# Performance work log

Hardware: AMD Instinct MI355X
Metric: run time of the kernel (lower is better)

The kernel has to match this reference:

```python
import jax, jax.numpy as jnp
import numpy as np

BN_EPS = 1e-5
K = 3  # k_size


def _unfold(x, k):
    # torch F.unfold with padding=k//2, stride=1, viewed as (B, C, k*k, H, W).
    # Kernel positions are row-major (i slow, j fast), matching torch layout.
    p = k // 2
    B, C, H, W = x.shape
    xp = jnp.pad(x, ((0, 0), (0, 0), (p, p), (p, p)))
    pats = jnp.stack([xp[:, :, i:i + H, j:j + W]
                      for i in range(k) for j in range(k)], axis=2)
    return pats  # (B, C, k*k, H, W)


def _conv1x1(x, w, b):
    # w: (C_out, C_in), x: (B, C_in, H, W)
    return jnp.einsum('oc,bchw->bohw', w, x) + b[None, :, None, None]


def _bn(x, gamma, beta, mean, var):
    inv = gamma / jnp.sqrt(var + BN_EPS)
    return x * inv[None, :, None, None] + (beta - mean * inv)[None, :, None, None]


def setup_inputs() -> dict:
    key = jax.random.key(0)
    ks = jax.random.split(key, 12)
    B, C, H, W = 8, 256, 64, 64
    s = lambda k_, *sh: jax.random.normal(k_, sh, dtype=jnp.float32) * 0.05
    return {
        'x': jax.random.normal(ks[0], (B, C, H, W), dtype=jnp.float32),
        # feature_embedding: Conv2d(C, C, 1) + BN
        'w_embed': s(ks[1], C, C), 'b_embed': jnp.zeros((C,), jnp.float32),
        'bn1_gamma': jnp.ones((C,), jnp.float32), 'bn1_beta': jnp.zeros((C,), jnp.float32),
        'bn1_mean': jnp.zeros((C,), jnp.float32), 'bn1_var': jnp.ones((C,), jnp.float32),
        # enhance: Conv2d(2C, C, 1) + BN
        'w_enh': s(ks[2], C, 2 * C), 'b_enh': jnp.zeros((C,), jnp.float32),
        'bn2_gamma': jnp.ones((C,), jnp.float32), 'bn2_beta': jnp.zeros((C,), jnp.float32),
        'bn2_mean': jnp.zeros((C,), jnp.float32), 'bn2_var': jnp.ones((C,), jnp.float32),
        # weight_gen: Conv2d(2C, C//4, 1) -> ReLU -> Conv2d(C//4, C, 1) -> Sigmoid
        'w_g1': s(ks[3], C // 4, 2 * C), 'b_g1': jnp.zeros((C // 4,), jnp.float32),
        'w_g2': s(ks[4], C, C // 4), 'b_g2': jnp.zeros((C,), jnp.float32),
    }


def reference(x, w_embed, b_embed, bn1_gamma, bn1_beta, bn1_mean, bn1_var,
              w_enh, b_enh, bn2_gamma, bn2_beta, bn2_mean, bn2_var,
              w_g1, b_g1, w_g2, b_g2):
    B, C, H, W = x.shape
    # ---- feature embedding: 1x1 conv + BN (eval) + ReLU
    fe = jax.nn.relu(_bn(_conv1x1(x, w_embed, b_embed),
                         bn1_gamma, bn1_beta, bn1_mean, bn1_var))
    # ---- region similarity: cosine(center pixel, each kxk neighbor) over C
    pats = _unfold(fe, K)                       # (B, C, k2, H, W)
    sim = jnp.einsum('bchw,bckhw->bkhw', fe, pats)
    norm_c = jnp.sqrt(jnp.sum(fe * fe, axis=1))             # (B, H, W)
    norm_p = jnp.sqrt(jnp.sum(pats * pats, axis=1))         # (B, k2, H, W)
    sim = sim / (norm_c[:, None] * norm_p + 1e-7)
    sim = jax.nn.softmax(sim, axis=1)                       # over k2 window
    # ---- dynamic feature aggregation on original x
    xpats = _unfold(x, K)                                   # (B, C, k2, H, W)
    agg = jnp.einsum('bckhw,bkhw->bchw', xpats, sim)
    enhanced = jax.nn.relu(_bn(_conv1x1(jnp.concatenate([x, agg], axis=1), w_enh, b_enh),
                               bn2_gamma, bn2_beta, bn2_mean, bn2_var))
    # ---- output modulation (SE-style gating)
    pooled = jnp.mean(jnp.concatenate([x, enhanced], axis=1), axis=(2, 3), keepdims=True)
    h = jax.nn.relu(_conv1x1(pooled, w_g1, b_g1))
    weights = jax.nn.sigmoid(_conv1x1(h, w_g2, b_g2))       # (B, C, 1, 1)
    return x + weights * enhanced
```

## Files before the change

kernel.cpp:

```cpp
#include <hip/hip_runtime.h>
#include <math.h>

typedef unsigned short u16;
typedef unsigned int   u32;
typedef __attribute__((ext_vector_type(8))) short short8;
typedef __attribute__((ext_vector_type(4))) float f32x4;

#define HW 4096

#define OFS_XB   0ul
#define OFS_PD   8388608ul
#define OFS_W1B  8683520ul
#define OFS_W2B  8716288ul
#define OFS_B1   8781824ul
#define OFS_B2   8782080ul
#define OFS_POOL 8782336ul
#define OFS_GATE 8786432ul
#define OFS_ENH  8788480ul

__device__ __forceinline__ u16 f2bf(float x) {
    union { float f; u32 u; } v; v.f = x;
    u32 r = v.u + 0x7fffu + ((v.u >> 16) & 1u);
    return (u16)(r >> 16);
}
__device__ __forceinline__ float bf2f(u16 h) {
    union { u32 u; float f; } v; v.u = ((u32)h) << 16;
    return v.f;
}
__device__ __forceinline__ void ld_g2l_16(u16* l, const u16* g) {
    __builtin_amdgcn_global_load_lds(
        (const __attribute__((address_space(1))) u32*)g,
        (__attribute__((address_space(3))) u32*)l,
        16, 0, 0);
}

__global__ __launch_bounds__(256) void k_cvt(
    const float* __restrict__ x, u16* __restrict__ xb, float* __restrict__ pool,
    const float* __restrict__ w1, const float* __restrict__ b1,
    const float* __restrict__ g1, const float* __restrict__ be1,
    const float* __restrict__ m1, const float* __restrict__ v1,
    const float* __restrict__ w2, const float* __restrict__ b2,
    const float* __restrict__ g2, const float* __restrict__ be2,
    const float* __restrict__ m2, const float* __restrict__ v2,
    u16* __restrict__ w1b, u16* __restrict__ w2b,
    float* __restrict__ b1f, float* __restrict__ b2f,
    float* __restrict__ pd)
{
    __shared__ float tile[64][65];
    const int t = threadIdx.x;
    const int id = blockIdx.x;
    if (id >= 2048) {
        const int pidb = id - 2048;
        if (pidb >= 770) {
            const int zid = pidb - 770;
            const float4 z = {0.f, 0.f, 0.f, 0.f};
            if (zid < 288) ((float4*)(pd + zid * 1024))[t] = z;
            else           ((float4*)(pool + (zid - 288) * 1024))[t] = z;
            return;
        }
        int idx = pidb * 256 + t;
        if (idx < 65536) {
            int o = idx >> 8;
            float inv = g1[o] * rsqrtf(v1[o] + 1e-5f);
            w1b[idx] = f2bf(w1[idx] * inv);
        } else if (idx < 196608) {
            int j = idx - 65536;
            int o = j >> 9;
            float inv = g2[o] * rsqrtf(v2[o] + 1e-5f);
            w2b[j] = f2bf(w2[j] * inv);
        } else if (idx < 196864) {
            int o = idx - 196608;
            float inv = g1[o] * rsqrtf(v1[o] + 1e-5f);
            b1f[o] = b1[o] * inv + be1[o] - m1[o] * inv;
        } else if (idx < 197120) {
            int o = idx - 196864;
            float inv = g2[o] * rsqrtf(v2[o] + 1e-5f);
            b2f[o] = b2[o] * inv + be2[o] - m2[o] * inv;
        }
        return;
    }
    const int pt = id & 63, ct = (id >> 6) & 3, b = id >> 8;
    const float* src = x + (((size_t)(b * 256 + ct * 64)) << 12) + pt * 64;
#pragma unroll
    for (int i = 0; i < 16; ++i) {
        int idx = i * 256 + t;
        int cl = idx >> 6, pl = idx & 63;
        tile[cl][pl] = src[((size_t)cl << 12) + pl];
    }
    __syncthreads();
#pragma unroll
    for (int i = 0; i < 8; ++i) {
        int idx = i * 256 + t;
        int pl = idx >> 5, c2 = idx & 31;
        int cl = c2 * 2;
        u32 lo = f2bf(tile[cl][pl]);
        u32 hi = f2bf(tile[cl + 1][pl]);
        u32 pv = lo | (hi << 16);
        *(u32*)(xb + (((size_t)(b * 4096 + pt * 64 + pl)) << 9) + ct * 64 + cl) = pv;
    }
    if (t < 64) {
        float s = 0.f;
#pragma unroll
        for (int i = 0; i < 64; ++i) s += tile[t][i];
        atomicAdd(&pool[(b << 9) + ct * 64 + t], s * (1.f / 4096.f));
    }
}

template<int KIN, bool OUTBF, bool DOPOOL>
__global__ __launch_bounds__(256) void k_gemm(
    const u16* __restrict__ xb, const u16* __restrict__ Wb,
    const float* __restrict__ biasf, void* __restrict__ outp,
    float* __restrict__ poolp)
{
    __shared__ __align__(16) u16 Wl[4096];
    __shared__ __align__(16) u16 Xl[4096];
    __shared__ float sbias[128];
    const int t = threadIdx.x;
    const int lane = t & 63;
    const int wv = t >> 6;
    const int p_blk = blockIdx.y * 128;
    const int o_blk = blockIdx.x * 128;
    const int owg = (wv & 1) * 4;
    const int pwg = (wv >> 1) * 4;
    const int r16 = lane & 15, q = lane >> 4;
    if (t < 128) sbias[t] = biasf[o_blk + t];

    f32x4 acc[4][4];
#pragma unroll
    for (int i = 0; i < 4; ++i)
#pragma unroll
        for (int j = 0; j < 4; ++j) acc[i][j] = (f32x4){0.f, 0.f, 0.f, 0.f};

    for (int kc = 0; kc < KIN / 32; ++kc) {
        const int kk = kc * 32 + q * 8;
#pragma unroll
        for (int s = 0; s < 4; ++s) {
            const int bi = wv * 4 + s;
            const u16* g;
            u16* l;
            if (bi < 8) {
                g = Wb + (size_t)(o_blk + bi * 16 + r16) * KIN + kk;
                l = Wl + bi * 512;
            } else {
                g = xb + (((size_t)(p_blk + (bi - 8) * 16 + r16)) << 9) + kk;
                l = Xl + (bi - 8) * 512;
            }
            ld_g2l_16(l, g);
        }
        __syncthreads();
        short8 af[4], bf[4];
#pragma unroll
        for (int i = 0; i < 4; ++i) af[i] = *(const short8*)(Wl + (owg + i) * 512 + lane * 8);
#pragma unroll
        for (int j = 0; j < 4; ++j) bf[j] = *(const short8*)(Xl + (pwg + j) * 512 + lane * 8);
#pragma unroll
        for (int i = 0; i < 4; ++i)
#pragma unroll
            for (int j = 0; j < 4; ++j)
                acc[i][j] = __builtin_amdgcn_mfma_f32_16x16x32_bf16(af[i], bf[j], acc[i][j], 0, 0, 0);
        __syncthreads();
    }

    float bia[4][4];
#pragma unroll
    for (int i = 0; i < 4; ++i)
#pragma unroll
        for (int r = 0; r < 4; ++r) bia[i][r] = sbias[owg * 16 + i * 16 + q * 4 + r];
    const int bidx = p_blk >> 12;
    const int pin0 = (p_blk & 4095) + pwg * 16 + r16;
#pragma unroll
    for (int i = 0; i < 4; ++i) {
#pragma unroll
        for (int r = 0; r < 4; ++r) {
            const int o = o_blk + owg * 16 + i * 16 + q * 4 + r;
            const size_t rowb = ((size_t)(bidx * 256 + o)) << 12;
            float ps = 0.f;
#pragma unroll
            for (int j = 0; j < 4; ++j) {
                float v = fmaxf(acc[i][j][r] + bia[i][r], 0.f);
                const size_t oi = rowb + pin0 + j * 16;
                if (OUTBF) ((u16*)outp)[oi] = f2bf(v);
                else       ((float*)outp)[oi] = v;
                ps += v;
            }
            if (DOPOOL) {
                ps += __shfl_down(ps, 8, 16);
                ps += __shfl_down(ps, 4, 16);
                ps += __shfl_down(ps, 2, 16);
                ps += __shfl_down(ps, 1, 16);
                if (r16 == 0)
                    atomicAdd(&poolp[(bidx << 9) + 256 + o], ps * (1.f / 4096.f));
            }
        }
    }
}

__global__ __launch_bounds__(256) void k_sim(
    const u16* __restrict__ fe, float* __restrict__ pd)
{
    __shared__ __align__(16) u16 st[3 * 4096];
    __shared__ float red[4][64][9];
    const int t = threadIdx.x;
    const int id = blockIdx.x;
    const int g = id & 3, h = (id >> 2) & 63, b = id >> 8;
    const int rows[3] = {h > 0 ? h - 1 : 0, h, h < 63 ? h + 1 : 63};
    const u16* base = fe + (((size_t)(b * 256 + g * 64)) << 12);
#pragma unroll
    for (int it = 0; it < 6; ++it) {
        const int flat = it * 256 + t;
        const int r = flat >> 9, j = flat & 511;
        const u16* gs = base + ((size_t)(j >> 3) << 12) + rows[r] * 64 + (j & 7) * 8;
        ld_g2l_16(st + r * 4096 + j * 8, gs);
    }
    __syncthreads();
    const int w = t & 63, sl = t >> 6;
    const int wl = w > 0 ? w - 1 : 0, wr = w < 63 ? w + 1 : 63;
    float dot[9] = {};
    const u16* s0 = st + sl * 16 * 64;
#pragma unroll 4
    for (int ci = 0; ci < 16; ++ci) {
        const u16* pc = s0 + ci * 64;
        float v[9];
#pragma unroll
        for (int r = 0; r < 3; ++r) {
            v[r * 3 + 0] = bf2f(pc[r * 4096 + wl]);
            v[r * 3 + 1] = bf2f(pc[r * 4096 + w]);
            v[r * 3 + 2] = bf2f(pc[r * 4096 + wr]);
        }
        const float c0 = v[4];
#pragma unroll
        for (int k = 0; k < 9; ++k) dot[k] = fmaf(c0, v[k], dot[k]);
    }
#pragma unroll
    for (int k = 0; k < 9; ++k) red[sl][w][k] = dot[k];
    __syncthreads();
    if (t < 64) {
        const int p = h * 64 + w;
#pragma unroll
        for (int k = 0; k < 9; ++k) {
            float s = red[0][w][k] + red[1][w][k] + red[2][w][k] + red[3][w][k];
            atomicAdd(&pd[((size_t)(b * 9 + k) << 12) + p], s);
        }
    }
}

__global__ __launch_bounds__(256) void k_agg(
    const u16* __restrict__ xb, const float* __restrict__ pd,
    u16* __restrict__ xbo)
{
    __shared__ __align__(16) u16 xt[3 * 4096];
    __shared__ float ws9[9][64];
    const int t = threadIdx.x;
    const int id = blockIdx.x;
    const int g = id & 3, h = (id >> 2) & 63, b = id >> 8;
    const int rows[3] = {h > 0 ? h - 1 : 0, h, h < 63 ? h + 1 : 63};
    const u16* base = xb + (((size_t)(b * 4096)) << 9) + g * 64;
#pragma unroll
    for (int it = 0; it < 6; ++it) {
        const int flat = it * 256 + t;
        const int r = flat >> 9, j = flat & 511;
        const u16* gs = base + (((size_t)(rows[r] * 64 + (j >> 3))) << 9) + (j & 7) * 8;
        ld_g2l_16(xt + r * 4096 + j * 8, gs);
    }
    if (t < 64) {
        const int w = t;
        const int p = h * 64 + w;
        const float* pb = pd + (((size_t)(b * 9)) << 12);
        const float nc = sqrtf(pb[(4 << 12) + p]);
        float s[9], mk[9];
#pragma unroll
        for (int di = -1; di <= 1; ++di)
#pragma unroll
            for (int dj = -1; dj <= 1; ++dj) {
                const int k = (di + 1) * 3 + (dj + 1);
                const int hn = h + di, wn = w + dj;
                const float mask = (hn >= 0 && hn < 64 && wn >= 0 && wn < 64) ? 1.f : 0.f;
                const int hc = hn < 0 ? 0 : (hn > 63 ? 63 : hn);
                const int wc = wn < 0 ? 0 : (wn > 63 ? 63 : wn);
                const float nk = pb[(4 << 12) + hc * 64 + wc];
                const float dk = pb[(k << 12) + p];
                mk[k] = mask;
                s[k] = mask * dk / (nc * sqrtf(nk) + 1e-7f);
            }
        float mx = s[0];
#pragma unroll
        for (int k = 1; k < 9; ++k) mx = fmaxf(mx, s[k]);
        float e[9], sum = 0.f;
#pragma unroll
        for (int k = 0; k < 9; ++k) { e[k] = expf(s[k] - mx); sum += e[k]; }
        const float rs = 1.f / sum;
#pragma unroll
        for (int k = 0; k < 9; ++k) ws9[k][w] = mk[k] * e[k] * rs;
    }
    __syncthreads();
    const int c = t & 63, pg = t >> 6;
    u16* orow = xbo + (((size_t)(b * 4096 + h * 64)) << 9) + 256 + g * 64 + c;
#pragma unroll 4
    for (int pi = 0; pi < 16; ++pi) {
        const int px = pg * 16 + pi;
        const int pl = px > 0 ? px - 1 : 0, pr = px < 63 ? px + 1 : 63;
        const int pxs[3] = {pl, px, pr};
        float m[9];
#pragma unroll
        for (int k = 0; k < 9; ++k) m[k] = ws9[k][px];
        float acc = 0.f;
#pragma unroll
        for (int r = 0; r < 3; ++r)
#pragma unroll
            for (int j = 0; j < 3; ++j)
                acc = fmaf(bf2f(xt[r * 4096 + pxs[j] * 64 + c]), m[r * 3 + j], acc);
        orow[(size_t)px << 9] = f2bf(acc);
    }
}

__global__ __launch_bounds__(64) void k_mlp(
    const float* __restrict__ pool,
    const float* __restrict__ wg1, const float* __restrict__ bg1,
    const float* __restrict__ wg2, const float* __restrict__ bg2,
    float* __restrict__ gate)
{
    __shared__ float pl[512];
    __shared__ float hb[64];
    const int b = blockIdx.x, t = threadIdx.x;
    for (int i = t; i < 512; i += 64) pl[i] = pool[b * 512 + i];
    __syncthreads();
    float s = bg1[t];
    const float* wr = wg1 + t * 512;
    for (int c = 0; c < 512; ++c) s = fmaf(wr[c], pl[c], s);
    hb[t] = fmaxf(s, 0.f);
    __syncthreads();
#pragma unroll
    for (int rr = 0; rr < 4; ++rr) {
        const int o = t + rr * 64;
        float s2 = bg2[o];
        const float* w2 = wg2 + o * 64;
        for (int j = 0; j < 64; ++j) s2 = fmaf(w2[j], hb[j], s2);
        gate[b * 256 + o] = 1.f / (1.f + expf(-s2));
    }
}

__global__ __launch_bounds__(256) void k_final(
    const u16* __restrict__ xb, const u16* __restrict__ enh,
    const float* __restrict__ gate, float* __restrict__ out)
{
    const int t = threadIdx.x;
    const int id = blockIdx.x;
    const int b = id >> 6, rg = id & 63;
    const int w = t & 63, s = t >> 6;
    const int p = rg * 64 + w;
    const u16* xrow = xb + (((size_t)(b * 4096 + p)) << 9) + s * 64;
#pragma unroll 2
    for (int cc = 0; cc < 8; ++cc) {
        short8 xv = *(const short8*)(xrow + cc * 8);
#pragma unroll
        for (int u = 0; u < 8; ++u) {
            const int c = s * 64 + cc * 8 + u;
            const float gt = gate[(b << 8) + c];
            const size_t off = (((size_t)(b * 256 + c)) << 12) + p;
            out[off] = fmaf(gt, bf2f(enh[off]), bf2f((u16)xv[u]));
        }
    }
}

extern "C" void kernel_launch(void* const* d_in, const int* in_sizes, int n_in,
                              void* d_out, int out_size, void* d_ws, size_t ws_size,
                              hipStream_t stream)
{
    const float* x       = (const float*)d_in[0];
    const float* w_embed = (const float*)d_in[1];
    const float* b_embed = (const float*)d_in[2];
    const float* g1      = (const float*)d_in[3];
    const float* be1     = (const float*)d_in[4];
    const float* m1      = (const float*)d_in[5];
    const float* v1      = (const float*)d_in[6];
    const float* w_enh   = (const float*)d_in[7];
    const float* b_enh   = (const float*)d_in[8];
    const float* g2      = (const float*)d_in[9];
    const float* be2     = (const float*)d_in[10];
    const float* m2      = (const float*)d_in[11];
    const float* v2      = (const float*)d_in[12];
    const float* w_g1    = (const float*)d_in[13];
    const float* b_g1    = (const float*)d_in[14];
    const float* w_g2    = (const float*)d_in[15];
    const float* b_g2    = (const float*)d_in[16];
    float* ws  = (float*)d_ws;
    float* out = (float*)d_out;

    u16*   xb   = (u16*)(ws + OFS_XB);
    float* pd   = ws + OFS_PD;
    u16*   w1b  = (u16*)(ws + OFS_W1B);
    u16*   w2b  = (u16*)(ws + OFS_W2B);
    float* b1f  = ws + OFS_B1;
    float* b2f  = ws + OFS_B2;
    float* pool = ws + OFS_POOL;
    float* gate = ws + OFS_GATE;
    u16*   enh  = (u16*)(ws + OFS_ENH);
    u16*   fe   = (u16*)d_out;

    k_cvt<<<dim3(3110), dim3(256), 0, stream>>>(
        x, xb, pool,
        w_embed, b_embed, g1, be1, m1, v1,
        w_enh, b_enh, g2, be2, m2, v2, w1b, w2b, b1f, b2f, pd);
    k_gemm<256, true, false><<<dim3(2, 256), dim3(256), 0, stream>>>(xb, w1b, b1f, (void*)fe, nullptr);
    k_sim<<<dim3(2048), dim3(256), 0, stream>>>(fe, pd);
    k_agg<<<dim3(2048), dim3(256), 0, stream>>>(xb, pd, xb);
    k_gemm<512, true, true><<<dim3(2, 256), dim3(256), 0, stream>>>(xb, w2b, b2f, (void*)enh, pool);
    k_mlp<<<dim3(8), dim3(64), 0, stream>>>(pool, w_g1, b_g1, w_g2, b_g2, gate);
    k_final<<<dim3(512), dim3(256), 0, stream>>>(xb, enh, gate, out);
}
```

Baseline: 215.1 us.

## Remap block indices across kernels and widen the gate MLP to 256 threads

Block-to-work mapping changes in several kernels. The GEMM uses a 1D grid that interleaves pixel and output tiles so neighbouring blocks share input and weight tiles. The sim, agg and final kernels put the batch index in the fastest-varying block bits. The convert kernel now dispatches its zeroing and weight-prep blocks first. The gate MLP runs with 256 threads, splitting the first matvec into four partial sums and giving each thread one output of the second. These aim to improve cache locality and XCD spread and to shorten the serial MLP, at the cost of changed memory access patterns that could hurt locality in the stencil kernels.

```diff
diff --git a/kernel.cpp b/kernel.cpp
--- a/kernel.cpp
+++ b/kernel.cpp
@@ -49,16 +49,14 @@
     __shared__ float tile[64][65];
     const int t = threadIdx.x;
     const int id = blockIdx.x;
-    if (id >= 2048) {
-        const int pidb = id - 2048;
-        if (pidb >= 770) {
-            const int zid = pidb - 770;
-            const float4 z = {0.f, 0.f, 0.f, 0.f};
-            if (zid < 288) ((float4*)(pd + zid * 1024))[t] = z;
-            else           ((float4*)(pool + (zid - 288) * 1024))[t] = z;
-            return;
-        }
-        int idx = pidb * 256 + t;
+    if (id < 292) {
+        const float4 z = {0.f, 0.f, 0.f, 0.f};
+        if (id < 288) ((float4*)(pd + id * 1024))[t] = z;
+        else          ((float4*)(pool + (id - 288) * 1024))[t] = z;
+        return;
+    }
+    if (id < 1062) {
+        int idx = (id - 292) * 256 + t;
         if (idx < 65536) {
             int o = idx >> 8;
             float inv = g1[o] * rsqrtf(v1[o] + 1e-5f);
@@ -79,7 +77,8 @@
         }
         return;
     }
-    const int pt = id & 63, ct = (id >> 6) & 3, b = id >> 8;
+    const int cid = id - 1062;
+    const int pt = cid & 63, ct = (cid >> 6) & 3, b = cid >> 8;
     const float* src = x + (((size_t)(b * 256 + ct * 64)) << 12) + pt * 64;
 #pragma unroll
     for (int i = 0; i < 16; ++i) {
@@ -95,8 +94,7 @@
         int cl = c2 * 2;
         u32 lo = f2bf(tile[cl][pl]);
         u32 hi = f2bf(tile[cl + 1][pl]);
-        u32 pv = lo | (hi << 16);
-        *(u32*)(xb + (((size_t)(b * 4096 + pt * 64 + pl)) << 9) + ct * 64 + cl) = pv;
+        *(u32*)(xb + (((size_t)(b * 4096 + pt * 64 + pl)) << 9) + ct * 64 + cl) = lo | (hi << 16);
     }
     if (t < 64) {
         float s = 0.f;
@@ -118,8 +116,9 @@
     const int t = threadIdx.x;
     const int lane = t & 63;
     const int wv = t >> 6;
-    const int p_blk = blockIdx.y * 128;
-    const int o_blk = blockIdx.x * 128;
+    const int id = blockIdx.x;
+    const int p_blk = (((id >> 4) << 3) | (id & 7)) * 128;
+    const int o_blk = ((id >> 3) & 1) * 128;
     const int owg = (wv & 1) * 4;
     const int pwg = (wv >> 1) * 4;
     const int r16 = lane & 15, q = lane >> 4;
@@ -179,8 +178,7 @@
             for (int j = 0; j < 4; ++j) {
                 float v = fmaxf(acc[i][j][r] + bia[i][r], 0.f);
                 const size_t oi = rowb + pin0 + j * 16;
-                if (OUTBF) ((u16*)outp)[oi] = f2bf(v);
-                else       ((float*)outp)[oi] = v;
+                ((u16*)outp)[oi] = f2bf(v);
                 ps += v;
             }
             if (DOPOOL) {
@@ -202,7 +200,7 @@
     __shared__ float red[4][64][9];
     const int t = threadIdx.x;
     const int id = blockIdx.x;
-    const int g = id & 3, h = (id >> 2) & 63, b = id >> 8;
+    const int b = id & 7, h = (id >> 3) & 63, g = id >> 9;
     const int rows[3] = {h > 0 ? h - 1 : 0, h, h < 63 ? h + 1 : 63};
     const u16* base = fe + (((size_t)(b * 256 + g * 64)) << 12);
 #pragma unroll
@@ -252,7 +250,7 @@
     __shared__ float ws9[9][64];
     const int t = threadIdx.x;
     const int id = blockIdx.x;
-    const int g = id & 3, h = (id >> 2) & 63, b = id >> 8;
+    const int b = id & 7, h = (id >> 3) & 63, g = id >> 9;
     const int rows[3] = {h > 0 ? h - 1 : 0, h, h < 63 ? h + 1 : 63};
     const u16* base = xb + (((size_t)(b * 4096)) << 9) + g * 64;
 #pragma unroll
@@ -313,30 +311,35 @@
     }
 }
 
-__global__ __launch_bounds__(64) void k_mlp(
+__global__ __launch_bounds__(256) void k_mlp(
     const float* __restrict__ pool,
     const float* __restrict__ wg1, const float* __restrict__ bg1,
     const float* __restrict__ wg2, const float* __restrict__ bg2,
     float* __restrict__ gate)
 {
     __shared__ float pl[512];
+    __shared__ float hpart[4][64];
     __shared__ float hb[64];
     const int b = blockIdx.x, t = threadIdx.x;
-    for (int i = t; i < 512; i += 64) pl[i] = pool[b * 512 + i];
-    __syncthreads();
-    float s = bg1[t];
-    const float* wr = wg1 + t * 512;
-    for (int c = 0; c < 512; ++c) s = fmaf(wr[c], pl[c], s);
-    hb[t] = fmaxf(s, 0.f);
-    __syncthreads();
-#pragma unroll
-    for (int rr = 0; rr < 4; ++rr) {
-        const int o = t + rr * 64;
-        float s2 = bg2[o];
-        const float* w2 = wg2 + o * 64;
-        for (int j = 0; j < 64; ++j) s2 = fmaf(w2[j], hb[j], s2);
-        gate[b * 256 + o] = 1.f / (1.f + expf(-s2));
-    }
+    pl[t] = pool[b * 512 + t];
+    pl[t + 256] = pool[b * 512 + t + 256];
+    __syncthreads();
+    const int o = t & 63, seg = t >> 6;
+    float s = 0.f;
+    const float* wr = wg1 + o * 512 + seg * 128;
+    const float* pr = pl + seg * 128;
+#pragma unroll 4
+    for (int j = 0; j < 128; ++j) s = fmaf(wr[j], pr[j], s);
+    hpart[seg][o] = s;
+    __syncthreads();
+    if (t < 64)
+        hb[t] = fmaxf(hpart[0][t] + hpart[1][t] + hpart[2][t] + hpart[3][t] + bg1[t], 0.f);
+    __syncthreads();
+    float s2 = bg2[t];
+    const float* w2 = wg2 + t * 64;
+#pragma unroll 4
+    for (int j = 0; j < 64; ++j) s2 = fmaf(w2[j], hb[j], s2);
+    gate[b * 256 + t] = 1.f / (1.f + expf(-s2));
 }
 
 __global__ __launch_bounds__(256) void k_final(
@@ -345,7 +348,7 @@
 {
     const int t = threadIdx.x;
     const int id = blockIdx.x;
-    const int b = id >> 6, rg = id & 63;
+    const int b = id & 7, rg = id >> 3;
     const int w = t & 63, s = t >> 6;
     const int p = rg * 64 + w;
     const u16* xrow = xb + (((size_t)(b * 4096 + p)) << 9) + s * 64;
@@ -401,10 +404,10 @@
         x, xb, pool,
         w_embed, b_embed, g1, be1, m1, v1,
         w_enh, b_enh, g2, be2, m2, v2, w1b, w2b, b1f, b2f, pd);
-    k_gemm<256, true, false><<<dim3(2, 256), dim3(256), 0, stream>>>(xb, w1b, b1f, (void*)fe, nullptr);
+    k_gemm<256, true, false><<<dim3(512), dim3(256), 0, stream>>>(xb, w1b, b1f, (void*)fe, nullptr);
     k_sim<<<dim3(2048), dim3(256), 0, stream>>>(fe, pd);
     k_agg<<<dim3(2048), dim3(256), 0, stream>>>(xb, pd, xb);
-    k_gemm<512, true, true><<<dim3(2, 256), dim3(256), 0, stream>>>(xb, w2b, b2f, (void*)enh, pool);
-    k_mlp<<<dim3(8), dim3(64), 0, stream>>>(pool, w_g1, b_g1, w_g2, b_g2, gate);
+    k_gemm<512, true, true><<<dim3(512), dim3(256), 0, stream>>>(xb, w2b, b2f, (void*)enh, pool);
+    k_mlp<<<dim3(8), dim3(256), 0, stream>>>(pool, w_g1, b_g1, w_g2, b_g2, gate);
     k_final<<<dim3(512), dim3(256), 0, stream>>>(xb, enh, gate, out);
 }
```

New measurement: 202.9 us. 5.7% less time.
